# Performance work log

Measured on AMD Instinct MI355X. Metric: run time of the kernel, lower is better.

The kernel has to match this reference:

```python
import jax, jax.numpy as jnp
import numpy as np

THRESHOLD = 1.0  # max tolerable Sampson error (px^2), as in the docstring example scale


def _normalize(pts, w):
    # pts: (B, M, 3) homogeneous points, w: (B, M) 0/1 weights.
    # Hartley normalization: centroid -> origin, mean distance -> sqrt(2).
    ws = w.sum(-1, keepdims=True)                                   # (B, 1)
    mean = (pts[..., :2] * w[..., None]).sum(-2) / ws               # (B, 2)
    d = jnp.linalg.norm(pts[..., :2] - mean[..., None, :], axis=-1)  # (B, M)
    md = (d * w).sum(-1) / ws[..., 0]                               # (B,)
    s = jnp.sqrt(2.0) / (md + 1e-8)
    z, o = jnp.zeros_like(s), jnp.ones_like(s)
    T = jnp.stack([
        jnp.stack([s, z, -s * mean[..., 0]], -1),
        jnp.stack([z, s, -s * mean[..., 1]], -1),
        jnp.stack([z, z, o], -1)], -2)                              # (B, 3, 3)
    return pts @ jnp.swapaxes(T, -1, -2), T


def eight_point(p1, p2, w):
    # Weighted normalized 8-point algorithm. p1, p2: (B, M, 3); w: (B, M).
    # Zero-weight rows contribute nothing to A^T A, so this equals fitting on the
    # selected subset (as the original does by fancy-indexing inlier rows).
    p1n, T1 = _normalize(p1, w)
    p2n, T2 = _normalize(p2, w)
    A = (p2n[..., :, None] * p1n[..., None, :]).reshape(p1.shape[:-2] + (-1, 9))
    A = A * w[..., None]                                            # (B, M, 9)
    AtA = jnp.einsum('...mi,...mj->...ij', A, A)                    # (B, 9, 9)
    _, V = jnp.linalg.eigh(AtA)                                     # ascending eigvals
    F = V[..., :, 0].reshape(p1.shape[:-2] + (3, 3))                # null vector
    U, S, Vt = jnp.linalg.svd(F, full_matrices=False)               # enforce rank 2
    F = (U * S.at[..., -1].set(0.0)[..., None, :]) @ Vt
    F = jnp.swapaxes(T2, -1, -2) @ F @ T1                           # denormalize
    return F / F[..., 2:3, 2:3]


def sampson_error(p1, p2, F):
    # p1, p2: (N, 3); F: (B, 3, 3) -> err: (B, N)
    Fx1 = jnp.einsum('bij,nj->bni', F, p1)
    Ftx2 = jnp.einsum('bij,ni->bnj', F, p2)
    num = jnp.einsum('ni,bni->bn', p2, Fx1) ** 2
    den = Fx1[..., 0] ** 2 + Fx1[..., 1] ** 2 + Ftx2[..., 0] ** 2 + Ftx2[..., 1] ** 2
    return num / den


def setup_inputs() -> dict:
    N, ITERS, K = 16384, 4096, 8
    rng = np.random.default_rng(0)
    X = rng.uniform(-2.0, 2.0, (N, 3)); X[:, 2] += 6.0               # 3D points, depth ~[4, 8]
    Kmat = np.array([[500.0, 0.0, 256.0], [0.0, 500.0, 256.0], [0.0, 0.0, 1.0]])
    th = 0.1
    R = np.array([[np.cos(th), 0.0, np.sin(th)], [0.0, 1.0, 0.0], [-np.sin(th), 0.0, np.cos(th)]])
    t = np.array([0.5, 0.1, 0.0])
    x1 = X @ Kmat.T; x1 /= x1[:, 2:]
    X2 = X @ R.T + t
    x2 = X2 @ Kmat.T; x2 /= x2[:, 2:]
    x1[:, :2] += rng.normal(0.0, 0.3, (N, 2))
    x2[:, :2] += rng.normal(0.0, 0.3, (N, 2))
    out = rng.random(N) < 0.3
    x2[out, :2] = rng.uniform(0.0, 512.0, (int(out.sum()), 2))
    samples = jax.random.randint(jax.random.key(0), (ITERS, K), 0, N, dtype=jnp.int32)
    return {"pts1": jnp.asarray(x1, jnp.float32), "pts2": jnp.asarray(x2, jnp.float32),
            "samples": samples, "iterations": ITERS, "num_of_select": K}


def reference(pts1, pts2, samples, iterations, num_of_select):
    samples = samples[:iterations, :num_of_select]                   # (B, 8), static slice
    # uniqueness check per hypothesis row (original drops non-unique rows; we mask them)
    srt = jnp.sort(samples, axis=-1)
    uniq = jnp.all(srt[:, 1:] != srt[:, :-1], axis=-1)               # (B,)
    p1s, p2s = pts1[samples], pts2[samples]                          # (B, 8, 3)
    w1 = jnp.ones(samples.shape, pts1.dtype)
    F = eight_point(p1s, p2s, w1)                                    # (B, 3, 3)
    err = sampson_error(pts1, pts2, F)                               # (B, N)
    inl = err <= THRESHOLD
    ml = inl.sum(-1).astype(pts1.dtype)                              # mask_lens
    ml_max = jnp.max(jnp.where(uniq, ml, 0.0))
    mask_len_ratio = ml / ml_max
    # sqrt of inlier errors; safe-guard masked entries so sqrt grad stays finite
    sqrt_sum = (jnp.sqrt(jnp.where(inl, err, 1.0)) * inl).sum(-1)
    means = (sqrt_sum + 1e-8) / (ml + 1e-8)
    means_max = jnp.max(jnp.where(uniq, means, -jnp.inf))
    score = 0.5 * mask_len_ratio + 0.5 * (1.0 - means / means_max)
    best = jnp.argmax(jnp.where(uniq, score, -jnp.inf))
    wbest = inl[best].astype(pts1.dtype)                             # (N,)
    Mbest = eight_point(pts1[None], pts2[None], wbest[None])[0]      # refit on inliers
    return Mbest, inl[best]
```

## Files before the change

kernel.cpp:

```cpp
#include <hip/hip_runtime.h>
#include <math.h>
#include <type_traits>
#include <utility>

#if defined(__has_builtin)
#if __has_builtin(__builtin_amdgcn_rcpf)
#define FAST_RCPF(x) __builtin_amdgcn_rcpf(x)
#endif
#if __has_builtin(__builtin_amdgcn_rsqf)
#define FAST_RSQF(x) __builtin_amdgcn_rsqf(x)
#endif
#endif
#ifndef FAST_RCPF
#define FAST_RCPF(x) (1.0f / (x))
#endif
#ifndef FAST_RSQF
#define FAST_RSQF(x) (1.0f / sqrtf(x))
#endif

__host__ __device__ constexpr int PIX(int i, int j) { return i * (i + 1) / 2 + j; }

template <int N, int I = 0, typename F>
__device__ __forceinline__ void static_for(F&& f) {
  if constexpr (I < N) {
    f(std::integral_constant<int, I>{});
    static_for<N, I + 1>(static_cast<F&&>(f));
  }
}

template <int I, int J, int K>
__device__ __forceinline__ double csub9(const double* M, double s) {
  if constexpr (K >= J) return s;
  else return csub9<I, J, K + 1>(M, s - M[PIX(I, K)] * M[PIX(J, K)]);
}
template <int I, int J>
__device__ __forceinline__ void cholJ(double* M) {
  if constexpr (J <= I) {
    double s = csub9<I, J, 0>(M, M[PIX(I, J)]);
    if constexpr (J == I)
      M[PIX(I, I)] = sqrt(fmax(s, 1e-300));
    else
      M[PIX(I, J)] = s / M[PIX(J, J)];
    cholJ<I, J + 1>(M);
  }
}
template <int I>
__device__ __forceinline__ void cholI(double* M) {
  if constexpr (I < 9) {
    cholJ<I, 0>(M);
    cholI<I + 1>(M);
  }
}

template <int I, int K>
__device__ __forceinline__ double fsub9(const double* L, const double* x, double s) {
  if constexpr (K >= I) return s;
  else return fsub9<I, K + 1>(L, x, s - L[PIX(I, K)] * x[K]);
}
template <int I>
__device__ __forceinline__ void fwd9(const double* L, double* x) {
  if constexpr (I < 9) {
    x[I] = fsub9<I, 0>(L, x, x[I]) / L[PIX(I, I)];
    fwd9<I + 1>(L, x);
  }
}
template <int I, int K>
__device__ __forceinline__ double bsub9(const double* L, const double* x, double s) {
  if constexpr (K >= 9) return s;
  else return bsub9<I, K + 1>(L, x, s - L[PIX(K, I)] * x[K]);
}
template <int I>
__device__ __forceinline__ void bwd9(const double* L, double* x) {
  if constexpr (I >= 0) {
    x[I] = bsub9<I, I + 1>(L, x, x[I]) / L[PIX(I, I)];
    bwd9<I - 1>(L, x);
  }
}

template <int I, int J>
__device__ __forceinline__ void ataIJ(double* M, const double (&a)[9], double w) {
  if constexpr (J <= I) {
    M[PIX(I, J)] += w * a[I] * a[J];
    ataIJ<I, J + 1>(M, a, w);
  }
}
template <int I>
__device__ __forceinline__ void ataI(double* M, const double (&a)[9], double w) {
  if constexpr (I < 9) {
    ataIJ<I, 0>(M, a, w);
    ataI<I + 1>(M, a, w);
  }
}

#define JROT(P, Q)                                                              \
  {                                                                             \
    double apq = a##P##Q;                                                       \
    if (fabs(apq) >= 1e-300) {                                                  \
      double tau = (a##Q##Q - a##P##P) / (2.0 * apq);                           \
      double t = ((tau >= 0.0) ? 1.0 : -1.0) / (fabs(tau) + sqrt(1.0 + tau * tau)); \
      double c = 1.0 / sqrt(1.0 + t * t);                                       \
      double s = t * c;                                                         \
      double t0p = a0##P, t0q = a0##Q;                                          \
      a0##P = c * t0p - s * t0q; a0##Q = s * t0p + c * t0q;                     \
      double t1p = a1##P, t1q = a1##Q;                                          \
      a1##P = c * t1p - s * t1q; a1##Q = s * t1p + c * t1q;                     \
      double t2p = a2##P, t2q = a2##Q;                                          \
      a2##P = c * t2p - s * t2q; a2##Q = s * t2p + c * t2q;                     \
      double rp0 = a##P##0, rq0 = a##Q##0;                                      \
      a##P##0 = c * rp0 - s * rq0; a##Q##0 = s * rp0 + c * rq0;                 \
      double rp1 = a##P##1, rq1 = a##Q##1;                                      \
      a##P##1 = c * rp1 - s * rq1; a##Q##1 = s * rp1 + c * rq1;                 \
      double rp2 = a##P##2, rq2 = a##Q##2;                                      \
      a##P##2 = c * rp2 - s * rq2; a##Q##2 = s * rp2 + c * rq2;                 \
      double u0p = V0##P, u0q = V0##Q;                                          \
      V0##P = c * u0p - s * u0q; V0##Q = s * u0p + c * u0q;                     \
      double u1p = V1##P, u1q = V1##Q;                                          \
      V1##P = c * u1p - s * u1q; V1##Q = s * u1p + c * u1q;                     \
      double u2p = V2##P, u2q = V2##Q;                                          \
      V2##P = c * u2p - s * u2q; V2##Q = s * u2p + c * u2q;                     \
    }                                                                           \
  }

__device__ __forceinline__ void solveF(double* M, double s1, double m1x, double m1y,
                                       double s2, double m2x, double m2y,
                                       float* out) {
  double tr = M[0] + M[2] + M[5] + M[9] + M[14] + M[20] + M[27] + M[35] + M[44];
  double shift = 1e-12 * tr;
  M[0] += shift; M[2] += shift; M[5] += shift; M[9] += shift; M[14] += shift;
  M[20] += shift; M[27] += shift; M[35] += shift; M[44] += shift;
  cholI<0>(M);
  double x[9];
  static_for<9>([&](auto i) { x[i] = 1.0; });
  static_for<3>([&](auto) {
    fwd9<0>(M, x);
    bwd9<8>(M, x);
    double n = 0.0;
    static_for<9>([&](auto i) { n += x[i] * x[i]; });
    n = 1.0 / sqrt(n);
    static_for<9>([&](auto i) { x[i] *= n; });
  });
  const double g00 = x[0] * x[0] + x[3] * x[3] + x[6] * x[6];
  const double g01 = x[0] * x[1] + x[3] * x[4] + x[6] * x[7];
  const double g02 = x[0] * x[2] + x[3] * x[5] + x[6] * x[8];
  const double g11 = x[1] * x[1] + x[4] * x[4] + x[7] * x[7];
  const double g12 = x[1] * x[2] + x[4] * x[5] + x[7] * x[8];
  const double g22 = x[2] * x[2] + x[5] * x[5] + x[8] * x[8];
  double a00 = g00, a01 = g01, a02 = g02;
  double a10 = g01, a11 = g11, a12 = g12;
  double a20 = g02, a21 = g12, a22 = g22;
  double V00 = 1, V01 = 0, V02 = 0;
  double V10 = 0, V11 = 1, V12 = 0;
  double V20 = 0, V21 = 0, V22 = 1;
  for (int sweep = 0; sweep < 6; ++sweep) {
    JROT(0, 1);
    JROT(0, 2);
    JROT(1, 2);
  }
  double mv = a00, v0 = V00, v1 = V10, v2 = V20;
  if (a11 < mv) { mv = a11; v0 = V01; v1 = V11; v2 = V21; }
  if (a22 < mv) { mv = a22; v0 = V02; v1 = V12; v2 = V22; }
  const double fv0 = x[0] * v0 + x[1] * v1 + x[2] * v2;
  const double fv1 = x[3] * v0 + x[4] * v1 + x[5] * v2;
  const double fv2 = x[6] * v0 + x[7] * v1 + x[8] * v2;
  const double F200 = x[0] - fv0 * v0, F201 = x[1] - fv0 * v1, F202 = x[2] - fv0 * v2;
  const double F210 = x[3] - fv1 * v0, F211 = x[4] - fv1 * v1, F212 = x[5] - fv1 * v2;
  const double F220 = x[6] - fv2 * v0, F221 = x[7] - fv2 * v1, F222 = x[8] - fv2 * v2;
  const double R00 = s2 * F200, R01 = s2 * F201, R02 = s2 * F202;
  const double R10 = s2 * F210, R11 = s2 * F211, R12 = s2 * F212;
  const double R20 = -s2 * m2x * F200 - s2 * m2y * F210 + F220;
  const double R21 = -s2 * m2x * F201 - s2 * m2y * F211 + F221;
  const double R22 = -s2 * m2x * F202 - s2 * m2y * F212 + F222;
  const double Ff00 = s1 * R00, Ff01 = s1 * R01;
  const double Ff02 = -s1 * m1x * R00 - s1 * m1y * R01 + R02;
  const double Ff10 = s1 * R10, Ff11 = s1 * R11;
  const double Ff12 = -s1 * m1x * R10 - s1 * m1y * R11 + R12;
  const double Ff20 = s1 * R20, Ff21 = s1 * R21;
  const double Ff22 = -s1 * m1x * R20 - s1 * m1y * R21 + R22;
  const double inv = 1.0 / Ff22;
  out[0] = (float)(Ff00 * inv); out[1] = (float)(Ff01 * inv); out[2] = (float)(Ff02 * inv);
  out[3] = (float)(Ff10 * inv); out[4] = (float)(Ff11 * inv); out[5] = (float)(Ff12 * inv);
  out[6] = (float)(Ff20 * inv); out[7] = (float)(Ff21 * inv); out[8] = (float)(Ff22 * inv);
}

struct F9 {
  float f0, f1, f2, f3, f4, f5, f6, f7, f8;
};

__device__ __forceinline__ F9 loadF(const float* __restrict__ p) {
  F9 F;
  F.f0 = p[0]; F.f1 = p[1]; F.f2 = p[2];
  F.f3 = p[3]; F.f4 = p[4]; F.f5 = p[5];
  F.f6 = p[6]; F.f7 = p[7]; F.f8 = p[8];
  return F;
}

__device__ __forceinline__ void samp_numden(const F9& F, float px, float py,
                                            float qx, float qy, float& num,
                                            float& den, float& dout) {
  float a0 = fmaf(F.f0, px, fmaf(F.f1, py, F.f2));
  float a1 = fmaf(F.f3, px, fmaf(F.f4, py, F.f5));
  float a2 = fmaf(F.f6, px, fmaf(F.f7, py, F.f8));
  float b0 = fmaf(F.f0, qx, fmaf(F.f3, qy, F.f6));
  float b1 = fmaf(F.f1, qx, fmaf(F.f4, qy, F.f7));
  float d = fmaf(qx, a0, fmaf(qy, a1, a2));
  num = d * d;
  den = fmaf(a0, a0, fmaf(a1, a1, fmaf(b0, b0, b1 * b1)));
  dout = d;
}

__device__ __forceinline__ void samp_acc(const F9& F, float px, float py,
                                         float qx, float qy, float& cnt,
                                         float& ss) {
  float num, den, d;
  samp_numden(F, px, py, qx, qy, num, den, d);
  const bool in = (num <= den);
  const float val = fabsf(d) * FAST_RSQF(den);
  cnt += in ? 1.0f : 0.0f;
  ss += in ? val : 0.0f;
}

__global__ __launch_bounds__(256, 1) void prep_and_fit(
    const float* __restrict__ pts1, const float* __restrict__ pts2,
    const int* __restrict__ samples, float2* __restrict__ P1,
    float2* __restrict__ P2, float* __restrict__ models,
    int* __restrict__ uflag, double* __restrict__ acc, int N, int iters,
    int TB) {
  if ((int)blockIdx.x < TB) {
    if (blockIdx.x == 0 && threadIdx.x < 52) acc[threadIdx.x] = 0.0;
    const int i = blockIdx.x * 256 + threadIdx.x;
    if (i < N) {
      P1[i] = make_float2(pts1[3 * i], pts1[3 * i + 1]);
      P2[i] = make_float2(pts2[3 * i], pts2[3 * i + 1]);
    }
    return;
  }
  if (threadIdx.x >= 64) return;
  const int it = (blockIdx.x - TB) * 64 + threadIdx.x;
  if (it >= iters) return;

  int idx[8];
  static_for<8>([&](auto k) { idx[k] = samples[it * 8 + k]; });
  int u = 1;
  static_for<8>([&](auto A) {
    static_for<8>([&](auto B) {
      if constexpr (decltype(B)::value > decltype(A)::value) {
        if (idx[A] == idx[B]) u = 0;
      }
    });
  });
  uflag[it] = u;

  float X1[8], Y1[8], Z1[8], X2[8], Y2[8], Z2[8];
  static_for<8>([&](auto k) {
    const int j = idx[k];
    X1[k] = pts1[3 * j]; Y1[k] = pts1[3 * j + 1]; Z1[k] = pts1[3 * j + 2];
    X2[k] = pts2[3 * j]; Y2[k] = pts2[3 * j + 1]; Z2[k] = pts2[3 * j + 2];
  });
  double sx1 = 0, sy1 = 0, sx2 = 0, sy2 = 0;
  static_for<8>([&](auto k) {
    sx1 += (double)X1[k]; sy1 += (double)Y1[k];
    sx2 += (double)X2[k]; sy2 += (double)Y2[k];
  });
  const double m1x = sx1 / 8.0, m1y = sy1 / 8.0;
  const double m2x = sx2 / 8.0, m2y = sy2 / 8.0;
  double sd1 = 0, sd2 = 0;
  static_for<8>([&](auto k) {
    double dx1 = (double)X1[k] - m1x, dy1 = (double)Y1[k] - m1y;
    double dx2 = (double)X2[k] - m2x, dy2 = (double)Y2[k] - m2y;
    sd1 += sqrt(dx1 * dx1 + dy1 * dy1);
    sd2 += sqrt(dx2 * dx2 + dy2 * dy2);
  });
  const double s1 = sqrt(2.0) / (sd1 / 8.0 + 1e-8);
  const double s2 = sqrt(2.0) / (sd2 / 8.0 + 1e-8);

  double M[45];
  static_for<45>([&](auto r) { M[r] = 0.0; });
  static_for<8>([&](auto k) {
    const double z1 = (double)Z1[k], z2 = (double)Z2[k];
    const double p1x = s1 * ((double)X1[k] - m1x * z1);
    const double p1y = s1 * ((double)Y1[k] - m1y * z1);
    const double p2x = s2 * ((double)X2[k] - m2x * z2);
    const double p2y = s2 * ((double)Y2[k] - m2y * z2);
    const double a[9] = {p2x * p1x, p2x * p1y, p2x * z1,
                         p2y * p1x, p2y * p1y, p2y * z1,
                         z2 * p1x,  z2 * p1y,  z2 * z1};
    ataI<0>(M, a, 1.0);
  });
  solveF(M, s1, m1x, m1y, s2, m2x, m2y, models + (size_t)it * 9);
}

__global__ __launch_bounds__(256, 4) void sampson_stats4(
    const float2* __restrict__ P1, const float2* __restrict__ P2,
    const float* __restrict__ models, float* __restrict__ ml,
    float* __restrict__ ssum, int N, int iters) {
  const int m0 = blockIdx.x * 4;
  const int c0 = min(m0 + 0, iters - 1), c1 = min(m0 + 1, iters - 1);
  const int c2 = min(m0 + 2, iters - 1), c3 = min(m0 + 3, iters - 1);
  const F9 Fa = loadF(models + (size_t)c0 * 9);
  const F9 Fb = loadF(models + (size_t)c1 * 9);
  const F9 Fc = loadF(models + (size_t)c2 * 9);
  const F9 Fd = loadF(models + (size_t)c3 * 9);
  float ca = 0, cb = 0, cc = 0, cd = 0;
  float sa = 0, sb = 0, sc_ = 0, sd = 0;
  const int NP = N & ~511;
  for (int i = threadIdx.x; i < NP; i += 512) {
    const float2 pA = P1[i];
    const float2 qA = P2[i];
    const float2 pB = P1[i + 256];
    const float2 qB = P2[i + 256];
    samp_acc(Fa, pA.x, pA.y, qA.x, qA.y, ca, sa);
    samp_acc(Fb, pA.x, pA.y, qA.x, qA.y, cb, sb);
    samp_acc(Fc, pA.x, pA.y, qA.x, qA.y, cc, sc_);
    samp_acc(Fd, pA.x, pA.y, qA.x, qA.y, cd, sd);
    samp_acc(Fa, pB.x, pB.y, qB.x, qB.y, ca, sa);
    samp_acc(Fb, pB.x, pB.y, qB.x, qB.y, cb, sb);
    samp_acc(Fc, pB.x, pB.y, qB.x, qB.y, cc, sc_);
    samp_acc(Fd, pB.x, pB.y, qB.x, qB.y, cd, sd);
  }
  for (int i = NP + threadIdx.x; i < N; i += 256) {
    const float2 p = P1[i];
    const float2 q = P2[i];
    samp_acc(Fa, p.x, p.y, q.x, q.y, ca, sa);
    samp_acc(Fb, p.x, p.y, q.x, q.y, cb, sb);
    samp_acc(Fc, p.x, p.y, q.x, q.y, cc, sc_);
    samp_acc(Fd, p.x, p.y, q.x, q.y, cd, sd);
  }
  __shared__ float shc[4][4], shs[4][4];
  const int lane = threadIdx.x & 63, wv = threadIdx.x >> 6;
  float c4[4] = {ca, cb, cc, cd};
  float s4[4] = {sa, sb, sc_, sd};
  static_for<4>([&](auto m) {
    float c = c4[m], s = s4[m];
#pragma unroll
    for (int o = 32; o > 0; o >>= 1) {
      c += __shfl_down(c, o);
      s += __shfl_down(s, o);
    }
    if (lane == 0) { shc[wv][m] = c; shs[wv][m] = s; }
  });
  __syncthreads();
  if (threadIdx.x < 4 && m0 + threadIdx.x < iters) {
    const int m = threadIdx.x;
    ml[m0 + m] = shc[0][m] + shc[1][m] + shc[2][m] + shc[3][m];
    ssum[m0 + m] = shs[0][m] + shs[1][m] + shs[2][m] + shs[3][m];
  }
}

__global__ __launch_bounds__(256) void selmask_p1(
    const float2* __restrict__ P1, const float2* __restrict__ P2,
    const float* __restrict__ models, const float* __restrict__ ml,
    const float* __restrict__ ssum, const int* __restrict__ uniq,
    float* __restrict__ outmask, double* __restrict__ acc, int N, int iters) {
  const int tid = threadIdx.x;
  __shared__ float ra[256], rb[256];
  __shared__ int rid[256];
  float mlmax = 0.f, mnmax = -INFINITY;
  for (int i = tid; i < iters; i += 256) {
    if (uniq[i]) {
      float m = ml[i];
      mlmax = fmaxf(mlmax, m);
      float mean = (ssum[i] + 1e-8f) / (m + 1e-8f);
      mnmax = fmaxf(mnmax, mean);
    }
  }
  ra[tid] = mlmax;
  rb[tid] = mnmax;
  __syncthreads();
  for (int s = 128; s > 0; s >>= 1) {
    if (tid < s) {
      ra[tid] = fmaxf(ra[tid], ra[tid + s]);
      rb[tid] = fmaxf(rb[tid], rb[tid + s]);
    }
    __syncthreads();
  }
  const float MLMAX = ra[0];
  const float MNMAX = rb[0];
  __syncthreads();
  float bsc = -INFINITY;
  int bid = 0x7FFFFFFF;
  for (int i = tid; i < iters; i += 256) {
    float sc = -INFINITY;
    float m = ml[i];
    float mean = (ssum[i] + 1e-8f) / (m + 1e-8f);
    if (uniq[i]) sc = 0.5f * (m / MLMAX) + 0.5f * (1.0f - mean / MNMAX);
    if (sc > bsc || (sc == bsc && i < bid)) { bsc = sc; bid = i; }
  }
  ra[tid] = bsc;
  rid[tid] = bid;
  __syncthreads();
  for (int s = 128; s > 0; s >>= 1) {
    if (tid < s) {
      if (ra[tid + s] > ra[tid] ||
          (ra[tid + s] == ra[tid] && rid[tid + s] < rid[tid])) {
        ra[tid] = ra[tid + s];
        rid[tid] = rid[tid + s];
      }
    }
    __syncthreads();
  }
  const int best = rid[0];

  const int i = blockIdx.x * 256 + tid;
  double w = 0, a = 0, b = 0, c = 0, d = 0;
  if (i < N) {
    const F9 F = loadF(models + (size_t)best * 9);
    const float2 p = P1[i];
    const float2 q = P2[i];
    float num, den, dd;
    samp_numden(F, p.x, p.y, q.x, q.y, num, den, dd);
    const bool in = (num <= den);
    float m = in ? 1.0f : 0.0f;
    outmask[i] = m;
    w = (double)m;
    a = w * (double)p.x;
    b = w * (double)p.y;
    c = w * (double)q.x;
    d = w * (double)q.y;
  }
#pragma unroll
  for (int o = 32; o > 0; o >>= 1) {
    w += __shfl_down(w, o); a += __shfl_down(a, o); b += __shfl_down(b, o);
    c += __shfl_down(c, o); d += __shfl_down(d, o);
  }
  if ((tid & 63) == 0) {
    atomicAdd(&acc[0], w); atomicAdd(&acc[1], a); atomicAdd(&acc[2], b);
    atomicAdd(&acc[3], c); atomicAdd(&acc[4], d);
  }
}

__global__ __launch_bounds__(256, 1) void ff_p23(
    const float* __restrict__ mask, const float2* __restrict__ P1,
    const float2* __restrict__ P2, double* __restrict__ acc, int N) {
  const double WS = acc[0];
  const double M1X = acc[1] / WS, M1Y = acc[2] / WS;
  const double M2X = acc[3] / WS, M2Y = acc[4] / WS;
  double sd1 = 0, sd2 = 0;
  double A[45];
  static_for<45>([&](auto r) { A[r] = 0.0; });
#pragma unroll
  for (int k = 0; k < 4; ++k) {
    const int i = blockIdx.x * 1024 + k * 256 + threadIdx.x;
    if (i < N) {
      const double w = (double)mask[i];
      if (w != 0.0) {
        const float2 p = P1[i];
        const float2 q = P2[i];
        const double v0 = (double)p.x - M1X, v1 = (double)p.y - M1Y;
        const double u0 = (double)q.x - M2X, u1 = (double)q.y - M2Y;
        sd1 += sqrt(v0 * v0 + v1 * v1);
        sd2 += sqrt(u0 * u0 + u1 * u1);
        const double a[9] = {u0 * v0, u0 * v1, u0,
                             u1 * v0, u1 * v1, u1,
                             v0,      v1,      1.0};
        ataI<0>(A, a, 1.0);
      }
    }
  }
  const int lane = threadIdx.x & 63;
  {
    double t1 = sd1, t2 = sd2;
#pragma unroll
    for (int o = 32; o > 0; o >>= 1) {
      t1 += __shfl_down(t1, o);
      t2 += __shfl_down(t2, o);
    }
    if (lane == 0) {
      atomicAdd(&acc[5], t1);
      atomicAdd(&acc[6], t2);
    }
  }
  static_for<45>([&](auto r) {
    double v = A[r];
#pragma unroll
    for (int o = 32; o > 0; o >>= 1) v += __shfl_down(v, o);
    if (lane == 0) atomicAdd(&acc[7 + r], v);
  });
}

__global__ __launch_bounds__(64, 1) void ff_solve(const double* __restrict__ acc,
                                                  float* __restrict__ outF) {
  if (threadIdx.x != 0 || blockIdx.x != 0) return;
  const double WS = acc[0];
  const double M1X = acc[1] / WS, M1Y = acc[2] / WS;
  const double M2X = acc[3] / WS, M2Y = acc[4] / WS;
  const double S1 = sqrt(2.0) / (acc[5] / WS + 1e-8);
  const double S2 = sqrt(2.0) / (acc[6] / WS + 1e-8);
  double M[45];
  static_for<45>([&](auto r) { M[r] = acc[7 + r]; });
  static_for<9>([&](auto R) {
    static_for<9>([&](auto C) {
      constexpr int r = decltype(R)::value;
      constexpr int c = decltype(C)::value;
      if constexpr (c <= r) {
        const double sr = ((r / 3) < 2 ? S2 : 1.0) * ((r % 3) < 2 ? S1 : 1.0);
        const double sc = ((c / 3) < 2 ? S2 : 1.0) * ((c % 3) < 2 ? S1 : 1.0);
        M[PIX(r, c)] *= sr * sc;
      }
    });
  });
  solveF(M, S1, M1X, M1Y, S2, M2X, M2Y, outF);
}

extern "C" void kernel_launch(void* const* d_in, const int* in_sizes, int n_in,
                              void* d_out, int out_size, void* d_ws, size_t ws_size,
                              hipStream_t stream) {
  const float* pts1 = (const float*)d_in[0];
  const float* pts2 = (const float*)d_in[1];
  const int* samples = (const int*)d_in[2];
  const int N = in_sizes[0] / 3;
  const int iters = in_sizes[2] / 8;

  float2* P1 = (float2*)d_ws;
  float2* P2 = P1 + N;
  double* acc = (double*)(P2 + N);
  float* models = (float*)(acc + 52);
  float* ml = models + (size_t)iters * 9;
  float* ssum = ml + iters;
  int* uniq = (int*)(ssum + iters);

  float* outF = (float*)d_out;
  float* outmask = outF + 9;

  const int TB = (N + 255) / 256;
  const int FB = (iters + 63) / 64;
  prep_and_fit<<<TB + FB, 256, 0, stream>>>(pts1, pts2, samples, P1, P2,
                                            models, uniq, acc, N, iters, TB);
  sampson_stats4<<<(iters + 3) / 4, 256, 0, stream>>>(P1, P2, models, ml, ssum,
                                                      N, iters);
  selmask_p1<<<(N + 255) / 256, 256, 0, stream>>>(P1, P2, models, ml, ssum,
                                                  uniq, outmask, acc, N, iters);
  ff_p23<<<(N + 1023) / 1024, 256, 0, stream>>>(outmask, P1, P2, acc, N);
  ff_solve<<<1, 64, 0, stream>>>(acc, outF);
}
```

Baseline: 179.2 us.

## Fuse mask, centroid, and raw-moment accumulation into one grid-synced kernel

Removes the separate ff_p23 kernel. The selection kernel now accumulates raw polynomial moments (products of monomials up to degree 2 in p and q) while the centroid is still unknown, then uses a last-block flag and spin-wait to publish the means so it can compute the distance sums. ff_solve turns the raw moments into the centered A^T A through binomial expansion. This saves one launch and one pass over the points, but it adds 36 wave-reductions with atomics per block and a grid-wide spin barrier that relies on all 64 blocks being co-resident. Expanding raw moments around the centroid may also lose precision through cancellation.

```diff
diff --git a/kernel.cpp b/kernel.cpp
--- a/kernel.cpp
+++ b/kernel.cpp
@@ -19,6 +19,19 @@
 #endif
 
 __host__ __device__ constexpr int PIX(int i, int j) { return i * (i + 1) / 2 + j; }
+
+__host__ __device__ constexpr int E1(int k) { return k == 1 ? 1 : k == 3 ? 2 : k == 4 ? 1 : 0; }
+__host__ __device__ constexpr int E2(int k) { return k == 2 ? 1 : k == 4 ? 1 : k == 5 ? 2 : 0; }
+__host__ __device__ constexpr int EIDX(int i, int j) {
+  return (i == 0 && j == 0) ? 0 : (i == 1 && j == 0) ? 1 : (i == 0 && j == 1) ? 2
+       : (i == 2 && j == 0) ? 3 : (i == 1 && j == 1) ? 4 : 5;
+}
+__host__ __device__ constexpr double BIN(int n, int k) { return (n == 2 && k == 1) ? 2.0 : 1.0; }
+template <int P>
+__device__ __forceinline__ double ipw(double x) {
+  if constexpr (P <= 0) return 1.0;
+  else return x * ipw<P - 1>(x);
+}
 
 template <int N, int I = 0, typename F>
 __device__ __forceinline__ void static_for(F&& f) {
@@ -223,10 +236,13 @@
     const float* __restrict__ pts1, const float* __restrict__ pts2,
     const int* __restrict__ samples, float2* __restrict__ P1,
     float2* __restrict__ P2, float* __restrict__ models,
-    int* __restrict__ uflag, double* __restrict__ acc, int N, int iters,
-    int TB) {
+    int* __restrict__ uflag, double* __restrict__ acc,
+    unsigned int* __restrict__ sync2, int N, int iters, int TB) {
   if ((int)blockIdx.x < TB) {
-    if (blockIdx.x == 0 && threadIdx.x < 52) acc[threadIdx.x] = 0.0;
+    if (blockIdx.x == 0) {
+      if (threadIdx.x < 48) acc[threadIdx.x] = 0.0;
+      if (threadIdx.x == 48) { sync2[0] = 0u; sync2[1] = 0u; }
+    }
     const int i = blockIdx.x * 256 + threadIdx.x;
     if (i < N) {
       P1[i] = make_float2(pts1[3 * i], pts1[3 * i + 1]);
@@ -346,11 +362,12 @@
   }
 }
 
-__global__ __launch_bounds__(256) void selmask_p1(
+__global__ __launch_bounds__(256, 1) void selmask_mom(
     const float2* __restrict__ P1, const float2* __restrict__ P2,
     const float* __restrict__ models, const float* __restrict__ ml,
     const float* __restrict__ ssum, const int* __restrict__ uniq,
-    float* __restrict__ outmask, double* __restrict__ acc, int N, int iters) {
+    float* __restrict__ outmask, double* __restrict__ acc,
+    unsigned int* __restrict__ sync2, int N, int iters, int NB) {
   const int tid = threadIdx.x;
   __shared__ float ra[256], rb[256];
   __shared__ int rid[256];
@@ -401,80 +418,101 @@
   const int best = rid[0];
 
   const int i = blockIdx.x * 256 + tid;
-  double w = 0, a = 0, b = 0, c = 0, d = 0;
+  float pxf = 0.f, pyf = 0.f, qxf = 0.f, qyf = 0.f;
+  bool in = false;
   if (i < N) {
     const F9 F = loadF(models + (size_t)best * 9);
     const float2 p = P1[i];
     const float2 q = P2[i];
+    pxf = p.x; pyf = p.y; qxf = q.x; qyf = q.y;
     float num, den, dd;
-    samp_numden(F, p.x, p.y, q.x, q.y, num, den, dd);
-    const bool in = (num <= den);
-    float m = in ? 1.0f : 0.0f;
-    outmask[i] = m;
-    w = (double)m;
-    a = w * (double)p.x;
-    b = w * (double)p.y;
-    c = w * (double)q.x;
-    d = w * (double)q.y;
+    samp_numden(F, pxf, pyf, qxf, qyf, num, den, dd);
+    in = (num <= den);
+    outmask[i] = in ? 1.0f : 0.0f;
+  }
+  const int lane = tid & 63;
+  const double px = (double)pxf, py = (double)pyf;
+  const double qx = (double)qxf, qy = (double)qyf;
+  {
+    double w = in ? 1.0 : 0.0;
+    double a = in ? px : 0.0, b = in ? py : 0.0;
+    double c = in ? qx : 0.0, d = in ? qy : 0.0;
+#pragma unroll
+    for (int o = 32; o > 0; o >>= 1) {
+      w += __shfl_down(w, o); a += __shfl_down(a, o); b += __shfl_down(b, o);
+      c += __shfl_down(c, o); d += __shfl_down(d, o);
+    }
+    if (lane == 0) {
+      atomicAdd(&acc[0], w); atomicAdd(&acc[1], a); atomicAdd(&acc[2], b);
+      atomicAdd(&acc[3], c); atomicAdd(&acc[4], d);
+    }
+  }
+  {
+    double um0 = 1.0, um1 = qx, um2 = qy, um3 = qx * qx, um4 = qx * qy,
+           um5 = qy * qy;
+    double vm0 = 1.0, vm1 = px, vm2 = py, vm3 = px * px, vm4 = px * py,
+           vm5 = py * py;
+    const double uu[6] = {um0, um1, um2, um3, um4, um5};
+    const double vv[6] = {vm0, vm1, vm2, vm3, vm4, vm5};
+    static_for<6>([&](auto QK) {
+      static_for<6>([&](auto PK) {
+        double prod = in ? uu[QK] * vv[PK] : 0.0;
+#pragma unroll
+        for (int o = 32; o > 0; o >>= 1) prod += __shfl_down(prod, o);
+        if (lane == 0)
+          atomicAdd(&acc[7 + decltype(QK)::value * 6 + decltype(PK)::value],
+                    prod);
+      });
+    });
+  }
+
+  __syncthreads();
+  __shared__ int amLast;
+  if (tid == 0) {
+    __threadfence();
+    amLast = (atomicAdd(&sync2[0], 1u) == (unsigned int)(NB - 1)) ? 1 : 0;
+  }
+  __syncthreads();
+  if (amLast && tid == 0) {
+    const double WS = atomicAdd(&acc[0], 0.0);
+    acc[43] = atomicAdd(&acc[1], 0.0) / WS;
+    acc[44] = atomicAdd(&acc[2], 0.0) / WS;
+    acc[45] = atomicAdd(&acc[3], 0.0) / WS;
+    acc[46] = atomicAdd(&acc[4], 0.0) / WS;
+    __threadfence();
+    atomicExch(&sync2[1], 1u);
+  }
+  __shared__ double smean[4];
+  if (tid == 0) {
+    while (atomicAdd(&sync2[1], 0u) == 0u) {
+      __builtin_amdgcn_s_sleep(1);
+    }
+    __threadfence();
+    smean[0] = atomicAdd(&acc[43], 0.0);
+    smean[1] = atomicAdd(&acc[44], 0.0);
+    smean[2] = atomicAdd(&acc[45], 0.0);
+    smean[3] = atomicAdd(&acc[46], 0.0);
+  }
+  __syncthreads();
+  const double M1X = smean[0], M1Y = smean[1];
+  const double M2X = smean[2], M2Y = smean[3];
+
+  double sd1 = 0, sd2 = 0;
+  if (in) {
+    const double v0 = px - M1X, v1 = py - M1Y;
+    const double u0 = qx - M2X, u1 = qy - M2Y;
+    sd1 = sqrt(v0 * v0 + v1 * v1);
+    sd2 = sqrt(u0 * u0 + u1 * u1);
   }
 #pragma unroll
   for (int o = 32; o > 0; o >>= 1) {
-    w += __shfl_down(w, o); a += __shfl_down(a, o); b += __shfl_down(b, o);
-    c += __shfl_down(c, o); d += __shfl_down(d, o);
-  }
-  if ((tid & 63) == 0) {
-    atomicAdd(&acc[0], w); atomicAdd(&acc[1], a); atomicAdd(&acc[2], b);
-    atomicAdd(&acc[3], c); atomicAdd(&acc[4], d);
-  }
-}
-
-__global__ __launch_bounds__(256, 1) void ff_p23(
-    const float* __restrict__ mask, const float2* __restrict__ P1,
-    const float2* __restrict__ P2, double* __restrict__ acc, int N) {
-  const double WS = acc[0];
-  const double M1X = acc[1] / WS, M1Y = acc[2] / WS;
-  const double M2X = acc[3] / WS, M2Y = acc[4] / WS;
-  double sd1 = 0, sd2 = 0;
-  double A[45];
-  static_for<45>([&](auto r) { A[r] = 0.0; });
-#pragma unroll
-  for (int k = 0; k < 4; ++k) {
-    const int i = blockIdx.x * 1024 + k * 256 + threadIdx.x;
-    if (i < N) {
-      const double w = (double)mask[i];
-      if (w != 0.0) {
-        const float2 p = P1[i];
-        const float2 q = P2[i];
-        const double v0 = (double)p.x - M1X, v1 = (double)p.y - M1Y;
-        const double u0 = (double)q.x - M2X, u1 = (double)q.y - M2Y;
-        sd1 += sqrt(v0 * v0 + v1 * v1);
-        sd2 += sqrt(u0 * u0 + u1 * u1);
-        const double a[9] = {u0 * v0, u0 * v1, u0,
-                             u1 * v0, u1 * v1, u1,
-                             v0,      v1,      1.0};
-        ataI<0>(A, a, 1.0);
-      }
-    }
-  }
-  const int lane = threadIdx.x & 63;
-  {
-    double t1 = sd1, t2 = sd2;
-#pragma unroll
-    for (int o = 32; o > 0; o >>= 1) {
-      t1 += __shfl_down(t1, o);
-      t2 += __shfl_down(t2, o);
-    }
-    if (lane == 0) {
-      atomicAdd(&acc[5], t1);
-      atomicAdd(&acc[6], t2);
-    }
-  }
-  static_for<45>([&](auto r) {
-    double v = A[r];
-#pragma unroll
-    for (int o = 32; o > 0; o >>= 1) v += __shfl_down(v, o);
-    if (lane == 0) atomicAdd(&acc[7 + r], v);
-  });
+    sd1 += __shfl_down(sd1, o);
+    sd2 += __shfl_down(sd2, o);
+  }
+  if (lane == 0) {
+    atomicAdd(&acc[5], sd1);
+    atomicAdd(&acc[6], sd2);
+  }
 }
 
 __global__ __launch_bounds__(64, 1) void ff_solve(const double* __restrict__ acc,
@@ -485,16 +523,56 @@
   const double M2X = acc[3] / WS, M2Y = acc[4] / WS;
   const double S1 = sqrt(2.0) / (acc[5] / WS + 1e-8);
   const double S2 = sqrt(2.0) / (acc[6] / WS + 1e-8);
+  double R[36];
+  static_for<36>([&](auto r) { R[r] = acc[7 + r]; });
+  double C[36];
+  static_for<6>([&](auto QP) {
+    static_for<6>([&](auto PP) {
+      constexpr int qp = decltype(QP)::value;
+      constexpr int pp = decltype(PP)::value;
+      constexpr int g1 = E1(qp), g2 = E2(qp), h1 = E1(pp), h2 = E2(pp);
+      double s = 0.0;
+      static_for<g1 + 1>([&](auto I_) {
+        static_for<g2 + 1>([&](auto J_) {
+          static_for<h1 + 1>([&](auto K_) {
+            static_for<h2 + 1>([&](auto L_) {
+              constexpr int ii = decltype(I_)::value;
+              constexpr int jj = decltype(J_)::value;
+              constexpr int kk = decltype(K_)::value;
+              constexpr int ll = decltype(L_)::value;
+              constexpr double bc =
+                  BIN(g1, ii) * BIN(g2, jj) * BIN(h1, kk) * BIN(h2, ll);
+              s += bc * ipw<g1 - ii>(-M2X) * ipw<g2 - jj>(-M2Y) *
+                   ipw<h1 - kk>(-M1X) * ipw<h2 - ll>(-M1Y) *
+                   R[EIDX(ii, jj) * 6 + EIDX(kk, ll)];
+            });
+          });
+        });
+      });
+      C[qp * 6 + pp] = s;
+    });
+  });
   double M[45];
-  static_for<45>([&](auto r) { M[r] = acc[7 + r]; });
-  static_for<9>([&](auto R) {
-    static_for<9>([&](auto C) {
-      constexpr int r = decltype(R)::value;
-      constexpr int c = decltype(C)::value;
-      if constexpr (c <= r) {
-        const double sr = ((r / 3) < 2 ? S2 : 1.0) * ((r % 3) < 2 ? S1 : 1.0);
-        const double sc = ((c / 3) < 2 ? S2 : 1.0) * ((c % 3) < 2 ? S1 : 1.0);
-        M[PIX(r, c)] *= sr * sc;
+  static_for<9>([&](auto I_) {
+    static_for<9>([&](auto J_) {
+      constexpr int i = decltype(I_)::value;
+      constexpr int j = decltype(J_)::value;
+      if constexpr (j <= i) {
+        constexpr int r = i / 3, c = i % 3, r2 = j / 3, c2 = j % 3;
+        constexpr int g1 = (r == 0) + (r2 == 0), g2 = (r == 1) + (r2 == 1);
+        constexpr int h1 = (c == 0) + (c2 == 0), h2 = (c == 1) + (c2 == 1);
+        M[PIX(i, j)] = C[EIDX(g1, g2) * 6 + EIDX(h1, h2)];
+      }
+    });
+  });
+  static_for<9>([&](auto I_) {
+    static_for<9>([&](auto J_) {
+      constexpr int i = decltype(I_)::value;
+      constexpr int j = decltype(J_)::value;
+      if constexpr (j <= i) {
+        const double sr = ((i / 3) < 2 ? S2 : 1.0) * ((i % 3) < 2 ? S1 : 1.0);
+        const double sc = ((j / 3) < 2 ? S2 : 1.0) * ((j % 3) < 2 ? S1 : 1.0);
+        M[PIX(i, j)] *= sr * sc;
       }
     });
   });
@@ -513,7 +591,8 @@
   float2* P1 = (float2*)d_ws;
   float2* P2 = P1 + N;
   double* acc = (double*)(P2 + N);
-  float* models = (float*)(acc + 52);
+  unsigned int* sync2 = (unsigned int*)(acc + 48);
+  float* models = (float*)(sync2 + 4);
   float* ml = models + (size_t)iters * 9;
   float* ssum = ml + iters;
   int* uniq = (int*)(ssum + iters);
@@ -523,12 +602,13 @@
 
   const int TB = (N + 255) / 256;
   const int FB = (iters + 63) / 64;
+  const int NB = (N + 255) / 256;
   prep_and_fit<<<TB + FB, 256, 0, stream>>>(pts1, pts2, samples, P1, P2,
-                                            models, uniq, acc, N, iters, TB);
+                                            models, uniq, acc, sync2, N,
+                                            iters, TB);
   sampson_stats4<<<(iters + 3) / 4, 256, 0, stream>>>(P1, P2, models, ml, ssum,
                                                       N, iters);
-  selmask_p1<<<(N + 255) / 256, 256, 0, stream>>>(P1, P2, models, ml, ssum,
-                                                  uniq, outmask, acc, N, iters);
-  ff_p23<<<(N + 1023) / 1024, 256, 0, stream>>>(outmask, P1, P2, acc, N);
+  selmask_mom<<<NB, 256, 0, stream>>>(P1, P2, models, ml, ssum, uniq, outmask,
+                                      acc, sync2, N, iters, NB);
   ff_solve<<<1, 64, 0, stream>>>(acc, outF);
 }
```

Result: slower. 220.2 us (+22.9%).

## Fuse inlier refit accumulation into selection kernel, replace atomics with partials

Applied to the files above, without the earlier changes.

The selection kernel now has every block redundantly recompute the inlier centroid over all N points. It then builds the 45 A^T A moments and the distance sums for its own slice and writes per-block partials instead of using double atomics. This removes the separate ff_p23 kernel, its launch and its global atomics, and ff_solve now reduces the partials. The cost is that each of the 64 blocks rescans all points to get the means, and each thread does 47 full wave shuffle reductions.

```diff
diff --git a/kernel.cpp b/kernel.cpp
--- a/kernel.cpp
+++ b/kernel.cpp
@@ -223,10 +223,8 @@
     const float* __restrict__ pts1, const float* __restrict__ pts2,
     const int* __restrict__ samples, float2* __restrict__ P1,
     float2* __restrict__ P2, float* __restrict__ models,
-    int* __restrict__ uflag, double* __restrict__ acc, int N, int iters,
-    int TB) {
+    int* __restrict__ uflag, int N, int iters, int TB) {
   if ((int)blockIdx.x < TB) {
-    if (blockIdx.x == 0 && threadIdx.x < 52) acc[threadIdx.x] = 0.0;
     const int i = blockIdx.x * 256 + threadIdx.x;
     if (i < N) {
       P1[i] = make_float2(pts1[3 * i], pts1[3 * i + 1]);
@@ -346,12 +344,14 @@
   }
 }
 
-__global__ __launch_bounds__(256) void selmask_p1(
+__global__ __launch_bounds__(256) void selmask_part(
     const float2* __restrict__ P1, const float2* __restrict__ P2,
     const float* __restrict__ models, const float* __restrict__ ml,
     const float* __restrict__ ssum, const int* __restrict__ uniq,
-    float* __restrict__ outmask, double* __restrict__ acc, int N, int iters) {
+    float* __restrict__ outmask, double* __restrict__ partials,
+    double* __restrict__ meanout, int N, int iters) {
   const int tid = threadIdx.x;
+  const int lane = tid & 63, wv = tid >> 6;
   __shared__ float ra[256], rb[256];
   __shared__ int rid[256];
   float mlmax = 0.f, mnmax = -INFINITY;
@@ -399,64 +399,80 @@
     __syncthreads();
   }
   const int best = rid[0];
+  const F9 F = loadF(models + (size_t)best * 9);
+
+  __shared__ double sm[5][4];
+  double sw = 0, spx = 0, spy = 0, sqx = 0, sqy = 0;
+  for (int i = tid; i < N; i += 256) {
+    const float2 p = P1[i];
+    const float2 q = P2[i];
+    float num, den, dd;
+    samp_numden(F, p.x, p.y, q.x, q.y, num, den, dd);
+    if (num <= den) {
+      sw += 1.0;
+      spx += (double)p.x;
+      spy += (double)p.y;
+      sqx += (double)q.x;
+      sqy += (double)q.y;
+    }
+  }
+  {
+    double v0 = sw, v1 = spx, v2 = spy, v3 = sqx, v4 = sqy;
+#pragma unroll
+    for (int o = 32; o > 0; o >>= 1) {
+      v0 += __shfl_down(v0, o); v1 += __shfl_down(v1, o);
+      v2 += __shfl_down(v2, o); v3 += __shfl_down(v3, o);
+      v4 += __shfl_down(v4, o);
+    }
+    if (lane == 0) {
+      sm[0][wv] = v0; sm[1][wv] = v1; sm[2][wv] = v2;
+      sm[3][wv] = v3; sm[4][wv] = v4;
+    }
+  }
+  __syncthreads();
+  const double WS = sm[0][0] + sm[0][1] + sm[0][2] + sm[0][3];
+  const double M1X = (sm[1][0] + sm[1][1] + sm[1][2] + sm[1][3]) / WS;
+  const double M1Y = (sm[2][0] + sm[2][1] + sm[2][2] + sm[2][3]) / WS;
+  const double M2X = (sm[3][0] + sm[3][1] + sm[3][2] + sm[3][3]) / WS;
+  const double M2Y = (sm[4][0] + sm[4][1] + sm[4][2] + sm[4][3]) / WS;
+  if (blockIdx.x == 0 && tid == 0) {
+    meanout[0] = WS;
+    meanout[1] = M1X; meanout[2] = M1Y;
+    meanout[3] = M2X; meanout[4] = M2Y;
+  }
+  __syncthreads();
 
   const int i = blockIdx.x * 256 + tid;
-  double w = 0, a = 0, b = 0, c = 0, d = 0;
+  double u0 = 0, u1 = 0, v0 = 0, v1 = 0, a8 = 0, sd1 = 0, sd2 = 0;
   if (i < N) {
-    const F9 F = loadF(models + (size_t)best * 9);
     const float2 p = P1[i];
     const float2 q = P2[i];
     float num, den, dd;
     samp_numden(F, p.x, p.y, q.x, q.y, num, den, dd);
     const bool in = (num <= den);
-    float m = in ? 1.0f : 0.0f;
-    outmask[i] = m;
-    w = (double)m;
-    a = w * (double)p.x;
-    b = w * (double)p.y;
-    c = w * (double)q.x;
-    d = w * (double)q.y;
-  }
+    outmask[i] = in ? 1.0f : 0.0f;
+    if (in) {
+      v0 = (double)p.x - M1X; v1 = (double)p.y - M1Y;
+      u0 = (double)q.x - M2X; u1 = (double)q.y - M2Y;
+      a8 = 1.0;
+      sd1 = sqrt(v0 * v0 + v1 * v1);
+      sd2 = sqrt(u0 * u0 + u1 * u1);
+    }
+  }
+  const double a[9] = {u0 * v0, u0 * v1, u0, u1 * v0, u1 * v1, u1, v0, v1, a8};
+  __shared__ double red[47][4];
+  static_for<9>([&](auto I_) {
+    static_for<9>([&](auto J_) {
+      constexpr int ii = decltype(I_)::value;
+      constexpr int jj = decltype(J_)::value;
+      if constexpr (jj <= ii) {
+        double v = a[ii] * a[jj];
 #pragma unroll
-  for (int o = 32; o > 0; o >>= 1) {
-    w += __shfl_down(w, o); a += __shfl_down(a, o); b += __shfl_down(b, o);
-    c += __shfl_down(c, o); d += __shfl_down(d, o);
-  }
-  if ((tid & 63) == 0) {
-    atomicAdd(&acc[0], w); atomicAdd(&acc[1], a); atomicAdd(&acc[2], b);
-    atomicAdd(&acc[3], c); atomicAdd(&acc[4], d);
-  }
-}
-
-__global__ __launch_bounds__(256, 1) void ff_p23(
-    const float* __restrict__ mask, const float2* __restrict__ P1,
-    const float2* __restrict__ P2, double* __restrict__ acc, int N) {
-  const double WS = acc[0];
-  const double M1X = acc[1] / WS, M1Y = acc[2] / WS;
-  const double M2X = acc[3] / WS, M2Y = acc[4] / WS;
-  double sd1 = 0, sd2 = 0;
-  double A[45];
-  static_for<45>([&](auto r) { A[r] = 0.0; });
-#pragma unroll
-  for (int k = 0; k < 4; ++k) {
-    const int i = blockIdx.x * 1024 + k * 256 + threadIdx.x;
-    if (i < N) {
-      const double w = (double)mask[i];
-      if (w != 0.0) {
-        const float2 p = P1[i];
-        const float2 q = P2[i];
-        const double v0 = (double)p.x - M1X, v1 = (double)p.y - M1Y;
-        const double u0 = (double)q.x - M2X, u1 = (double)q.y - M2Y;
-        sd1 += sqrt(v0 * v0 + v1 * v1);
-        sd2 += sqrt(u0 * u0 + u1 * u1);
-        const double a[9] = {u0 * v0, u0 * v1, u0,
-                             u1 * v0, u1 * v1, u1,
-                             v0,      v1,      1.0};
-        ataI<0>(A, a, 1.0);
+        for (int o = 32; o > 0; o >>= 1) v += __shfl_down(v, o);
+        if (lane == 0) red[PIX(ii, jj)][wv] = v;
       }
-    }
-  }
-  const int lane = threadIdx.x & 63;
+    });
+  });
   {
     double t1 = sd1, t2 = sd2;
 #pragma unroll
@@ -464,37 +480,42 @@
       t1 += __shfl_down(t1, o);
       t2 += __shfl_down(t2, o);
     }
-    if (lane == 0) {
-      atomicAdd(&acc[5], t1);
-      atomicAdd(&acc[6], t2);
-    }
-  }
-  static_for<45>([&](auto r) {
-    double v = A[r];
-#pragma unroll
-    for (int o = 32; o > 0; o >>= 1) v += __shfl_down(v, o);
-    if (lane == 0) atomicAdd(&acc[7 + r], v);
-  });
-}
-
-__global__ __launch_bounds__(64, 1) void ff_solve(const double* __restrict__ acc,
-                                                  float* __restrict__ outF) {
-  if (threadIdx.x != 0 || blockIdx.x != 0) return;
-  const double WS = acc[0];
-  const double M1X = acc[1] / WS, M1Y = acc[2] / WS;
-  const double M2X = acc[3] / WS, M2Y = acc[4] / WS;
-  const double S1 = sqrt(2.0) / (acc[5] / WS + 1e-8);
-  const double S2 = sqrt(2.0) / (acc[6] / WS + 1e-8);
+    if (lane == 0) { red[45][wv] = t1; red[46][wv] = t2; }
+  }
+  __syncthreads();
+  if (tid < 47) {
+    partials[(size_t)blockIdx.x * 48 + tid] =
+        red[tid][0] + red[tid][1] + red[tid][2] + red[tid][3];
+  }
+}
+
+__global__ __launch_bounds__(64, 1) void ff_solve(
+    const double* __restrict__ partials, const double* __restrict__ meanout,
+    float* __restrict__ outF, int NB) {
+  if (blockIdx.x != 0) return;
+  __shared__ double red[47];
+  if (threadIdx.x < 47) {
+    double s = 0.0;
+    for (int b = 0; b < NB; ++b) s += partials[(size_t)b * 48 + threadIdx.x];
+    red[threadIdx.x] = s;
+  }
+  __syncthreads();
+  if (threadIdx.x != 0) return;
+  const double WS = meanout[0];
+  const double M1X = meanout[1], M1Y = meanout[2];
+  const double M2X = meanout[3], M2Y = meanout[4];
+  const double S1 = sqrt(2.0) / (red[45] / WS + 1e-8);
+  const double S2 = sqrt(2.0) / (red[46] / WS + 1e-8);
   double M[45];
-  static_for<45>([&](auto r) { M[r] = acc[7 + r]; });
-  static_for<9>([&](auto R) {
-    static_for<9>([&](auto C) {
-      constexpr int r = decltype(R)::value;
-      constexpr int c = decltype(C)::value;
-      if constexpr (c <= r) {
-        const double sr = ((r / 3) < 2 ? S2 : 1.0) * ((r % 3) < 2 ? S1 : 1.0);
-        const double sc = ((c / 3) < 2 ? S2 : 1.0) * ((c % 3) < 2 ? S1 : 1.0);
-        M[PIX(r, c)] *= sr * sc;
+  static_for<45>([&](auto r) { M[r] = red[r]; });
+  static_for<9>([&](auto I_) {
+    static_for<9>([&](auto J_) {
+      constexpr int i = decltype(I_)::value;
+      constexpr int j = decltype(J_)::value;
+      if constexpr (j <= i) {
+        const double sr = ((i / 3) < 2 ? S2 : 1.0) * ((i % 3) < 2 ? S1 : 1.0);
+        const double sc = ((j / 3) < 2 ? S2 : 1.0) * ((j % 3) < 2 ? S1 : 1.0);
+        M[PIX(i, j)] *= sr * sc;
       }
     });
   });
@@ -510,10 +531,15 @@
   const int N = in_sizes[0] / 3;
   const int iters = in_sizes[2] / 8;
 
+  const int TB = (N + 255) / 256;
+  const int FB = (iters + 63) / 64;
+  const int NB = (N + 255) / 256;
+
   float2* P1 = (float2*)d_ws;
   float2* P2 = P1 + N;
-  double* acc = (double*)(P2 + N);
-  float* models = (float*)(acc + 52);
+  double* partials = (double*)(P2 + N);
+  double* meanout = partials + (size_t)NB * 48;
+  float* models = (float*)(meanout + 8);
   float* ml = models + (size_t)iters * 9;
   float* ssum = ml + iters;
   int* uniq = (int*)(ssum + iters);
@@ -521,14 +547,11 @@
   float* outF = (float*)d_out;
   float* outmask = outF + 9;
 
-  const int TB = (N + 255) / 256;
-  const int FB = (iters + 63) / 64;
   prep_and_fit<<<TB + FB, 256, 0, stream>>>(pts1, pts2, samples, P1, P2,
-                                            models, uniq, acc, N, iters, TB);
+                                            models, uniq, N, iters, TB);
   sampson_stats4<<<(iters + 3) / 4, 256, 0, stream>>>(P1, P2, models, ml, ssum,
                                                       N, iters);
-  selmask_p1<<<(N + 255) / 256, 256, 0, stream>>>(P1, P2, models, ml, ssum,
-                                                  uniq, outmask, acc, N, iters);
-  ff_p23<<<(N + 1023) / 1024, 256, 0, stream>>>(outmask, P1, P2, acc, N);
-  ff_solve<<<1, 64, 0, stream>>>(acc, outF);
-}
+  selmask_part<<<NB, 256, 0, stream>>>(P1, P2, models, ml, ssum, uniq,
+                                       outmask, partials, meanout, N, iters);
+  ff_solve<<<1, 64, 0, stream>>>(partials, meanout, outF, NB);
+}
```

Result: slower. 182.8 us (+2.0%).
